# Kernel optimization log

Measured on AMD Instinct MI355X. Metric: run time of the kernel, lower is better.

The kernel has to match this reference:

```python
import jax, jax.numpy as jnp
import numpy as np

N = 50000       # num_nodes
E = 800000      # num_edges (avg degree 16)
DIN = 128       # input_dim
DOUT = 128      # output_dim
H = 4           # num_heads
HD = DOUT // H  # head_dim = 32


def setup_inputs() -> dict:
    key = jax.random.key(0)
    ks = jax.random.split(key, 9)
    x = jax.random.normal(ks[0], (N, DIN), dtype=jnp.float32)
    edge_index = jax.random.randint(ks[1], (2, E), 0, N, dtype=jnp.int64)
    s = 1.0 / np.sqrt(DIN)
    Wq = jax.random.uniform(ks[2], (DOUT, DIN), jnp.float32, -s, s)
    bq = jax.random.uniform(ks[3], (DOUT,), jnp.float32, -s, s)
    Wk = jax.random.uniform(ks[4], (DOUT, DIN), jnp.float32, -s, s)
    bk = jax.random.uniform(ks[5], (DOUT,), jnp.float32, -s, s)
    Wv = jax.random.uniform(ks[6], (DOUT, DIN), jnp.float32, -s, s)
    bv = jax.random.uniform(ks[7], (DOUT,), jnp.float32, -s, s)
    att = jax.random.normal(ks[8], (H, 2 * HD), dtype=jnp.float32)  # nn.Parameter(randn)
    return {"x": x, "edge_index": edge_index, "Wq": Wq, "bq": bq,
            "Wk": Wk, "bk": bk, "Wv": Wv, "bv": bv, "att": att}


def reference(x, edge_index, Wq, bq, Wk, bk, Wv, bv, att):
    n = x.shape[0]
    q = (x @ Wq.T + bq).reshape(n, H, HD)
    k = (x @ Wk.T + bk).reshape(n, H, HD)
    v = (x @ Wv.T + bv).reshape(n, H, HD)
    row, col = edge_index[0], edge_index[1]

    # scores = leaky_relu(sum(cat([q[row],k[col]]) * att)) computed without concat
    a_q, a_k = att[:, :HD], att[:, HD:]                       # [H,HD] each
    scores = jnp.einsum('ehd,hd->eh', q[row], a_q) \
           + jnp.einsum('ehd,hd->eh', k[col], a_k)            # [E,H]
    scores = jax.nn.leaky_relu(scores, 0.2)

    # segment-softmax over edges grouped by destination node (col), per head
    m = jax.ops.segment_max(scores, col, num_segments=n)      # [N,H]
    m = jnp.where(jnp.isfinite(m), m, 0.0)                    # empty segments -> -inf guard
    e = jnp.exp(scores - m[col])                              # [E,H]
    denom = jax.ops.segment_sum(e, col, num_segments=n)       # [N,H]
    w_edge = e / denom[col]                                   # softmax per dst segment

    # attention_weights[i] = mean over incoming edges of softmax weights; 0 if deg==0
    deg = jax.ops.segment_sum(jnp.ones((col.shape[0],), jnp.float32), col,
                              num_segments=n)                 # [N]
    w_sum = jax.ops.segment_sum(w_edge, col, num_segments=n)  # [N,H]
    attn_w = jnp.where(deg[:, None] > 0, w_sum / jnp.maximum(deg, 1.0)[:, None], 0.0)

    # output[dst] += attn_w[dst] * v[src], summed over edges
    msgs = attn_w[col][:, :, None] * v[row]                   # [E,H,HD]
    out = jax.ops.segment_sum(msgs, col, num_segments=n)      # [N,H,HD]
    return out.reshape(n, DOUT)                               # dropout: eval mode (identity)
```

## Files before the change

kernel.cpp:

```cpp
#include <hip/hip_runtime.h>


#define N_NODES 50000
#define N_EDGES 800000
#define SPAN    96
#define NBUCK   521
#define CAP     2304
#define EPB     4096
#define NCHUNK  196

#define OFF_SORTED 12800000
#define OFF_CURSOR 17601536
#define OFF_FLAG   17603712
#define OFF_XH     17603840

typedef __attribute__((ext_vector_type(8))) short short8;
typedef __attribute__((ext_vector_type(4))) float f32x4;

__global__ void detect_kernel(const int* __restrict__ ei, int* __restrict__ flag) {
    int t = threadIdx.x;
    int nz = (ei[2 * t + 1] != 0) ? 1 : 0;
    unsigned long long b = __ballot(nz);
    if (t == 0) *flag = (b == 0ULL) ? 1 : 0;
}

__device__ __forceinline__ unsigned int pack_bf16_rne(float a, float b) {
    unsigned int ua = __float_as_uint(a), ub = __float_as_uint(b);
    unsigned int ha = (ua + 0x7FFFu + ((ua >> 16) & 1u)) >> 16;
    unsigned int hb = (ub + 0x7FFFu + ((ub >> 16) & 1u)) >> 16;
    return ha | (hb << 16);
}
__device__ __forceinline__ unsigned short bf16_rne(float a) {
    unsigned int ua = __float_as_uint(a);
    return (unsigned short)((ua + 0x7FFFu + ((ua >> 16) & 1u)) >> 16);
}

__global__ __launch_bounds__(256) void xconv_kernel(const float* __restrict__ x,
                                                    unsigned int* __restrict__ xh) {
    int i = blockIdx.x * 256 + threadIdx.x;
    if (i < (N_NODES * 128) / 4) {
        float4 v = ((const float4*)x)[i];
        uint2 o;
        o.x = pack_bf16_rne(v.x, v.y);
        o.y = pack_bf16_rne(v.z, v.w);
        ((uint2*)xh)[i] = o;
    }
}

__global__ __launch_bounds__(256) void gemm_v(const unsigned int* __restrict__ xh,
                                              const float* __restrict__ Wv,
                                              const float* __restrict__ bv,
                                              unsigned int* __restrict__ vh) {
    __shared__ __align__(16) unsigned int wB[128 * 68];
    int t = threadIdx.x;

    for (int q = t; q < 8192; q += 256) {
        int o = q >> 6, k2 = q & 63;
        float2 wp = ((const float2*)Wv)[q];
        wB[o * 68 + k2] = pack_bf16_rne(wp.x, wp.y);
    }
    __syncthreads();

    int lane = t & 63, w = t >> 6;
    int quad = lane >> 4, lc = lane & 15;
    int n0 = blockIdx.x * 64 + w * 16;

    int arow = n0 + lc;
    int arowc = min(arow, N_NODES - 1);
    const uint4* aptr = (const uint4*)(xh + (size_t)arowc * 64);

    f32x4 acc[8];
    #pragma unroll
    for (int ot = 0; ot < 8; ++ot) acc[ot] = (f32x4){0.f, 0.f, 0.f, 0.f};

    #pragma unroll
    for (int ks = 0; ks < 4; ++ks) {
        uint4 a4 = aptr[ks * 4 + quad];
        short8 af = *(const short8*)&a4;
        #pragma unroll
        for (int ot = 0; ot < 8; ++ot) {
            uint4 b4 = *(const uint4*)&wB[(ot * 16 + lc) * 68 + ks * 16 + quad * 4];
            short8 bf = *(const short8*)&b4;
            acc[ot] = __builtin_amdgcn_mfma_f32_16x16x32_bf16(af, bf, acc[ot], 0, 0, 0);
        }
    }

    #pragma unroll
    for (int ot = 0; ot < 8; ++ot) {
        int o = ot * 16 + lc;
        float bb = bv[o];
        #pragma unroll
        for (int r = 0; r < 4; ++r) {
            int node = n0 + quad * 4 + r;
            unsigned short u = bf16_rne(acc[ot][r] + bb);
            unsigned int partner = (unsigned int)__shfl_xor((int)u, 1, 64);
            if ((lane & 1) == 0 && node < N_NODES) {
                unsigned int pair = (unsigned int)u | (partner << 16);
                vh[(size_t)node * 64 + (o >> 1)] = pair;
            }
        }
    }
}

__global__ __launch_bounds__(512) void scatter_kernel(const int* __restrict__ ei,
                                                      const int* __restrict__ flag,
                                                      int* __restrict__ Cursor,
                                                      unsigned int* __restrict__ sorted) {
    __shared__ unsigned int w[EPB];
    __shared__ int h[NBUCK];
    __shared__ int base[NBUCK];
    int t = threadIdx.x;
    for (int j = t; j < NBUCK; j += 512) h[j] = 0;
    __syncthreads();
    int wide = *flag;
    int e0 = blockIdx.x * EPB;

    #pragma unroll
    for (int k = 0; k < EPB / 512; ++k) {
        int e = e0 + k * 512 + t;
        if (e < N_EDGES) {
            int r = wide ? ei[2 * e] : ei[e];
            int c = wide ? ei[2 * (N_EDGES + e)] : ei[N_EDGES + e];
            w[k * 512 + t] = ((unsigned int)c << 16) | (unsigned int)r;
            atomicAdd(&h[c / SPAN], 1);
        } else {
            w[k * 512 + t] = 0xFFFFFFFFu;
        }
    }
    __syncthreads();
    for (int j = t; j < NBUCK; j += 512) {
        int cnt = h[j];
        base[j] = cnt ? atomicAdd(&Cursor[j], cnt) : 0;
        h[j] = 0;
    }
    __syncthreads();
    #pragma unroll
    for (int k = 0; k < EPB / 512; ++k) {
        unsigned int ww = w[k * 512 + t];
        if (ww != 0xFFFFFFFFu) {
            int bin = (int)(ww >> 16) / SPAN;
            int p = base[bin] + atomicAdd(&h[bin], 1);
            if (p < CAP)
                sorted[(size_t)bin * CAP + p] = ww;
        }
    }
}

__global__ __launch_bounds__(512) void gather_kernel(const unsigned int* __restrict__ vh,
                                                     const unsigned int* __restrict__ sorted,
                                                     const int* __restrict__ Cursor,
                                                     float* __restrict__ out) {
    __shared__ int deg[SPAN];
    __shared__ int startc[SPAN];
    __shared__ int curp[SPAN];
    __shared__ int sc_s[128];
    __shared__ unsigned short rl[CAP];
    int t = threadIdx.x;
    int b = blockIdx.x;
    int nb0 = b * SPAN;
    int span = min(SPAN, N_NODES - nb0);
    int cnt = min(Cursor[b], CAP);
    if (t < SPAN) deg[t] = 0;
    __syncthreads();

    const unsigned int* run = sorted + (size_t)b * CAP;
    for (int i = t; i < cnt; i += 512) atomicAdd(&deg[(int)(run[i] >> 16) - nb0], 1);
    __syncthreads();

    if (t < 128) sc_s[t] = (t < SPAN) ? deg[t] : 0;
    __syncthreads();
    for (int off = 1; off < 128; off <<= 1) {
        int y = (t < 128 && t >= off) ? sc_s[t - off] : 0;
        __syncthreads();
        if (t < 128) sc_s[t] += y;
        __syncthreads();
    }
    if (t < SPAN) { startc[t] = sc_s[t] - deg[t]; curp[t] = 0; }
    __syncthreads();

    for (int i = t; i < cnt; i += 512) {
        unsigned int ww = run[i];
        int ln = (int)(ww >> 16) - nb0;
        int p = startc[ln] + atomicAdd(&curp[ln], 1);
        rl[p] = (unsigned short)(ww & 0xFFFFu);
    }
    __syncthreads();

    int lane = t & 63, wid = t >> 6;
    for (int ln = wid; ln < span; ln += 8) {
        int s0 = startc[ln], d = deg[ln];
        float ax = 0.f, ay = 0.f, bx = 0.f, by = 0.f;
        float cx = 0.f, cy = 0.f, dx = 0.f, dy = 0.f;
        int j = 0;
        for (; j + 4 <= d; j += 4) {
            int r0 = rl[s0 + j], r1 = rl[s0 + j + 1];
            int r2 = rl[s0 + j + 2], r3 = rl[s0 + j + 3];
            unsigned int p0 = vh[r0 * 64 + lane];
            unsigned int p1 = vh[r1 * 64 + lane];
            unsigned int p2 = vh[r2 * 64 + lane];
            unsigned int p3 = vh[r3 * 64 + lane];
            ax += __uint_as_float(p0 << 16); ay += __uint_as_float(p0 & 0xFFFF0000u);
            bx += __uint_as_float(p1 << 16); by += __uint_as_float(p1 & 0xFFFF0000u);
            cx += __uint_as_float(p2 << 16); cy += __uint_as_float(p2 & 0xFFFF0000u);
            dx += __uint_as_float(p3 << 16); dy += __uint_as_float(p3 & 0xFFFF0000u);
        }
        for (; j < d; ++j) {
            int r0 = rl[s0 + j];
            unsigned int p0 = vh[r0 * 64 + lane];
            ax += __uint_as_float(p0 << 16); ay += __uint_as_float(p0 & 0xFFFF0000u);
        }
        float sc = (d > 0) ? 1.0f / (float)d : 0.0f;
        float2 res;
        res.x = ((ax + bx) + (cx + dx)) * sc;
        res.y = ((ay + by) + (cy + dy)) * sc;
        ((float2*)out)[(size_t)(nb0 + ln) * 64 + lane] = res;
    }
}

extern "C" void kernel_launch(void* const* d_in, const int* in_sizes, int n_in,
                              void* d_out, int out_size, void* d_ws, size_t ws_size,
                              hipStream_t stream) {
    const float* x  = (const float*)d_in[0];
    const int*   ei = (const int*)d_in[1];
    const float* Wv = (const float*)d_in[6];
    const float* bv = (const float*)d_in[7];
    float* out = (float*)d_out;

    char* ws = (char*)d_ws;
    unsigned int* vh     = (unsigned int*)(ws);
    unsigned int* sorted = (unsigned int*)(ws + OFF_SORTED);
    int*          Cursor = (int*)(ws + OFF_CURSOR);
    int*          flag   = (int*)(ws + OFF_FLAG);
    unsigned int* xh     = (unsigned int*)(ws + OFF_XH);

    hipMemsetAsync(Cursor, 0, NBUCK * sizeof(int), stream);
    detect_kernel<<<1, 64, 0, stream>>>(ei, flag);
    xconv_kernel<<<(N_NODES * 128 / 4 + 255) / 256, 256, 0, stream>>>(x, xh);
    gemm_v<<<(N_NODES + 63) / 64, 256, 0, stream>>>(xh, Wv, bv, vh);
    scatter_kernel<<<NCHUNK, 512, 0, stream>>>(ei, flag, Cursor, sorted);
    gather_kernel<<<NBUCK, 512, 0, stream>>>(vh, sorted, Cursor, out);
}
```

Measured before the change: 157.2 us.

## Fuse bf16 conversion into GEMM, fold flag detection into scatter, shrink gather buckets

Drops the separate x-to-bf16 conversion kernel: the V projection GEMM now reads fp32 rows of x and packs them to bf16 in registers before the MFMA. The edge-index width check moves from its own kernel into each scatter block via a per-block ballot. Node buckets are halved (48 nodes, 1042 buckets, smaller capacity), and the gather kernel uses 256 threads and stages each bucket's run in LDS so global memory is read only once. The goal is fewer launches, no intermediate bf16 copy of x, and more gather blocks in flight. The cost is twice the fp32 x traffic per GEMM tile load and redundant flag detection in every scatter block.

```diff
diff --git a/kernel.cpp b/kernel.cpp
--- a/kernel.cpp
+++ b/kernel.cpp
@@ -3,26 +3,17 @@
 
 #define N_NODES 50000
 #define N_EDGES 800000
-#define SPAN    96
-#define NBUCK   521
-#define CAP     2304
+#define SPAN    48
+#define NBUCK   1042
+#define CAP     1152
 #define EPB     4096
 #define NCHUNK  196
 
 #define OFF_SORTED 12800000
 #define OFF_CURSOR 17601536
-#define OFF_FLAG   17603712
-#define OFF_XH     17603840
 
 typedef __attribute__((ext_vector_type(8))) short short8;
 typedef __attribute__((ext_vector_type(4))) float f32x4;
-
-__global__ void detect_kernel(const int* __restrict__ ei, int* __restrict__ flag) {
-    int t = threadIdx.x;
-    int nz = (ei[2 * t + 1] != 0) ? 1 : 0;
-    unsigned long long b = __ballot(nz);
-    if (t == 0) *flag = (b == 0ULL) ? 1 : 0;
-}
 
 __device__ __forceinline__ unsigned int pack_bf16_rne(float a, float b) {
     unsigned int ua = __float_as_uint(a), ub = __float_as_uint(b);
@@ -35,19 +26,7 @@
     return (unsigned short)((ua + 0x7FFFu + ((ua >> 16) & 1u)) >> 16);
 }
 
-__global__ __launch_bounds__(256) void xconv_kernel(const float* __restrict__ x,
-                                                    unsigned int* __restrict__ xh) {
-    int i = blockIdx.x * 256 + threadIdx.x;
-    if (i < (N_NODES * 128) / 4) {
-        float4 v = ((const float4*)x)[i];
-        uint2 o;
-        o.x = pack_bf16_rne(v.x, v.y);
-        o.y = pack_bf16_rne(v.z, v.w);
-        ((uint2*)xh)[i] = o;
-    }
-}
-
-__global__ __launch_bounds__(256) void gemm_v(const unsigned int* __restrict__ xh,
+__global__ __launch_bounds__(256) void gemm_v(const float* __restrict__ x,
                                               const float* __restrict__ Wv,
                                               const float* __restrict__ bv,
                                               unsigned int* __restrict__ vh) {
@@ -67,7 +46,7 @@
 
     int arow = n0 + lc;
     int arowc = min(arow, N_NODES - 1);
-    const uint4* aptr = (const uint4*)(xh + (size_t)arowc * 64);
+    const float4* xrow = (const float4*)(x + (size_t)arowc * 128);
 
     f32x4 acc[8];
     #pragma unroll
@@ -75,7 +54,13 @@
 
     #pragma unroll
     for (int ks = 0; ks < 4; ++ks) {
-        uint4 a4 = aptr[ks * 4 + quad];
+        float4 f0 = xrow[ks * 8 + quad * 2];
+        float4 f1 = xrow[ks * 8 + quad * 2 + 1];
+        uint4 a4;
+        a4.x = pack_bf16_rne(f0.x, f0.y);
+        a4.y = pack_bf16_rne(f0.z, f0.w);
+        a4.z = pack_bf16_rne(f1.x, f1.y);
+        a4.w = pack_bf16_rne(f1.z, f1.w);
         short8 af = *(const short8*)&a4;
         #pragma unroll
         for (int ot = 0; ot < 8; ++ot) {
@@ -103,16 +88,21 @@
 }
 
 __global__ __launch_bounds__(512) void scatter_kernel(const int* __restrict__ ei,
-                                                      const int* __restrict__ flag,
                                                       int* __restrict__ Cursor,
                                                       unsigned int* __restrict__ sorted) {
     __shared__ unsigned int w[EPB];
     __shared__ int h[NBUCK];
     __shared__ int base[NBUCK];
+    __shared__ int s_wide;
     int t = threadIdx.x;
     for (int j = t; j < NBUCK; j += 512) h[j] = 0;
-    __syncthreads();
-    int wide = *flag;
+    if (t < 64) {
+        int nz = (ei[2 * t + 1] != 0) ? 1 : 0;
+        unsigned long long b = __ballot(nz);
+        if (t == 0) s_wide = (b == 0ULL) ? 1 : 0;
+    }
+    __syncthreads();
+    int wide = s_wide;
     int e0 = blockIdx.x * EPB;
 
     #pragma unroll
@@ -146,15 +136,16 @@
     }
 }
 
-__global__ __launch_bounds__(512) void gather_kernel(const unsigned int* __restrict__ vh,
+__global__ __launch_bounds__(256) void gather_kernel(const unsigned int* __restrict__ vh,
                                                      const unsigned int* __restrict__ sorted,
                                                      const int* __restrict__ Cursor,
                                                      float* __restrict__ out) {
+    __shared__ unsigned int ww[CAP];
+    __shared__ unsigned short rl[CAP];
     __shared__ int deg[SPAN];
     __shared__ int startc[SPAN];
     __shared__ int curp[SPAN];
-    __shared__ int sc_s[128];
-    __shared__ unsigned short rl[CAP];
+    __shared__ int sc_s[64];
     int t = threadIdx.x;
     int b = blockIdx.x;
     int nb0 = b * SPAN;
@@ -164,30 +155,34 @@
     __syncthreads();
 
     const unsigned int* run = sorted + (size_t)b * CAP;
-    for (int i = t; i < cnt; i += 512) atomicAdd(&deg[(int)(run[i] >> 16) - nb0], 1);
-    __syncthreads();
-
-    if (t < 128) sc_s[t] = (t < SPAN) ? deg[t] : 0;
-    __syncthreads();
-    for (int off = 1; off < 128; off <<= 1) {
-        int y = (t < 128 && t >= off) ? sc_s[t - off] : 0;
+    for (int i = t; i < cnt; i += 256) {
+        unsigned int v = run[i];
+        ww[i] = v;
+        atomicAdd(&deg[(int)(v >> 16) - nb0], 1);
+    }
+    __syncthreads();
+
+    if (t < 64) sc_s[t] = (t < SPAN) ? deg[t] : 0;
+    __syncthreads();
+    for (int off = 1; off < 64; off <<= 1) {
+        int y = (t < 64 && t >= off) ? sc_s[t - off] : 0;
         __syncthreads();
-        if (t < 128) sc_s[t] += y;
+        if (t < 64) sc_s[t] += y;
         __syncthreads();
     }
     if (t < SPAN) { startc[t] = sc_s[t] - deg[t]; curp[t] = 0; }
     __syncthreads();
 
-    for (int i = t; i < cnt; i += 512) {
-        unsigned int ww = run[i];
-        int ln = (int)(ww >> 16) - nb0;
+    for (int i = t; i < cnt; i += 256) {
+        unsigned int v = ww[i];
+        int ln = (int)(v >> 16) - nb0;
         int p = startc[ln] + atomicAdd(&curp[ln], 1);
-        rl[p] = (unsigned short)(ww & 0xFFFFu);
+        rl[p] = (unsigned short)(v & 0xFFFFu);
     }
     __syncthreads();
 
     int lane = t & 63, wid = t >> 6;
-    for (int ln = wid; ln < span; ln += 8) {
+    for (int ln = wid; ln < span; ln += 4) {
         int s0 = startc[ln], d = deg[ln];
         float ax = 0.f, ay = 0.f, bx = 0.f, by = 0.f;
         float cx = 0.f, cy = 0.f, dx = 0.f, dy = 0.f;
@@ -230,13 +225,9 @@
     unsigned int* vh     = (unsigned int*)(ws);
     unsigned int* sorted = (unsigned int*)(ws + OFF_SORTED);
     int*          Cursor = (int*)(ws + OFF_CURSOR);
-    int*          flag   = (int*)(ws + OFF_FLAG);
-    unsigned int* xh     = (unsigned int*)(ws + OFF_XH);
 
     hipMemsetAsync(Cursor, 0, NBUCK * sizeof(int), stream);
-    detect_kernel<<<1, 64, 0, stream>>>(ei, flag);
-    xconv_kernel<<<(N_NODES * 128 / 4 + 255) / 256, 256, 0, stream>>>(x, xh);
-    gemm_v<<<(N_NODES + 63) / 64, 256, 0, stream>>>(xh, Wv, bv, vh);
-    scatter_kernel<<<NCHUNK, 512, 0, stream>>>(ei, flag, Cursor, sorted);
-    gather_kernel<<<NBUCK, 512, 0, stream>>>(vh, sorted, Cursor, out);
-}
+    gemm_v<<<(N_NODES + 63) / 64, 256, 0, stream>>>(x, Wv, bv, vh);
+    scatter_kernel<<<NCHUNK, 512, 0, stream>>>(ei, Cursor, sorted);
+    gather_kernel<<<NBUCK, 256, 0, stream>>>(vh, sorted, Cursor, out);
+}
```

New measurement: 156.6 us. Within noise of the previous version (-0.4%).
